# Kernel tuning notes

Measured on AMD Instinct MI355X. Metric: run time of the kernel, lower is better.

The kernel has to match this reference:

```python
import jax, jax.numpy as jnp
import numpy as np
from jax import lax

B, C, H, W = 4, 128, 64, 64
GC = 32        # branch channels = C * branch_ratio
DI = 64        # SS2D d_inner = 2 * GC (expand=2)
DT_RANK = 2    # ceil(GC / 16)


def _conv(x, w, pad, dilation=1, groups=1):
    return lax.conv_general_dilated(x, w, (1, 1), [(pad, pad), (pad, pad)],
                                    rhs_dilation=(dilation, dilation),
                                    feature_group_count=groups,
                                    dimension_numbers=('NCHW', 'OIHW', 'NCHW'))


def _bn(x, g, b, m, v):
    # inference-mode BatchNorm2d
    s = g / jnp.sqrt(v + 1e-5)
    return x * s[None, :, None, None] + (b - m * s)[None, :, None, None]


def _selective_scan(u, delta, A, Bm, Cm, D, dbias):
    # u, delta: (B,K,Di,L); A: (K,Di,N); Bm,Cm: (B,K,N,L); D,dbias: (K,Di)
    delta = jax.nn.softplus(delta + dbias[None, :, :, None])
    Bsz, K, Di, L = u.shape
    N = A.shape[-1]

    def step(h, inp):
        dt, bt, ct, ut = inp  # dt,ut: (B,K,Di); bt,ct: (B,K,N)
        h = jnp.exp(dt[..., None] * A) * h + (dt * ut)[..., None] * bt[:, :, None, :]
        return h, jnp.einsum('bkdn,bkn->bkd', h, ct)

    xs = (jnp.moveaxis(delta, -1, 0), jnp.moveaxis(Bm, -1, 0),
          jnp.moveaxis(Cm, -1, 0), jnp.moveaxis(u, -1, 0))
    _, ys = lax.scan(step, jnp.zeros((Bsz, K, Di, N), u.dtype), xs)
    return jnp.moveaxis(ys, 0, -1) + u * D[None, :, :, None]


def _ss2d(x, in_w, cw, cb, xp_w, dt_w, dt_b, A_log, Dp, ln_g, ln_b, out_w):
    # VMamba SS2D on NCHW input
    Bsz, Cc, Hh, Ww = x.shape
    di = in_w.shape[0] // 2
    dc = cw.shape[-1]
    xz = jnp.einsum('bchw,ec->behw', x, in_w)          # in_proj (bias=False)
    xi, z = jnp.split(xz, 2, axis=1)
    xc = jax.nn.silu(_conv(xi, cw, (dc - 1) // 2, groups=di) + cb[None, :, None, None])
    L = Hh * Ww
    xf = xc.reshape(Bsz, di, L)
    xt = xc.transpose(0, 1, 3, 2).reshape(Bsz, di, L)
    x2 = jnp.stack([xf, xt], 1)
    xs4 = jnp.concatenate([x2, jnp.flip(x2, -1)], 1)   # (B,4,di,L) cross-scan
    x_dbl = jnp.einsum('bkdl,kcd->bkcl', xs4, xp_w)
    r = dt_w.shape[-1]
    N = A_log.shape[-1]
    dts = jnp.einsum('bkrl,kdr->bkdl', x_dbl[:, :, :r], dt_w)
    Bs = x_dbl[:, :, r:r + N]
    Cs = x_dbl[:, :, r + N:]
    A = -jnp.exp(A_log).reshape(4, di, N)
    oy = _selective_scan(xs4, dts, A, Bs, Cs, Dp.reshape(4, di), dt_b)
    inv = jnp.flip(oy[:, 2:4], -1)
    wh = oy[:, 1].reshape(Bsz, di, Ww, Hh).transpose(0, 1, 3, 2).reshape(Bsz, di, L)
    iwh = inv[:, 1].reshape(Bsz, di, Ww, Hh).transpose(0, 1, 3, 2).reshape(Bsz, di, L)
    y = (oy[:, 0] + inv[:, 0] + wh + iwh).transpose(0, 2, 1).reshape(Bsz, Hh, Ww, di)
    mu = y.mean(-1, keepdims=True)
    y = (y - mu) * lax.rsqrt(((y - mu) ** 2).mean(-1, keepdims=True) + 1e-5) * ln_g + ln_b
    y = y * jax.nn.silu(z.transpose(0, 2, 3, 1))
    return jnp.einsum('bhwd,cd->bchw', y, out_w)


def _gcss2d(x, in_w, cw, cb, xp_w, dt_w, dt_b, A_log, Dp, ln_g, ln_b, out_w, pw, bg, bb, bm, bv):
    s = _ss2d(x, in_w, cw, cb, xp_w, dt_w, dt_b, A_log, Dp, ln_g, ln_b, out_w)
    # AdaptiveAvgPool2d(1) + bilinear upsample of a 1x1 map == broadcast
    pool = jnp.broadcast_to(x.mean((2, 3), keepdims=True), s.shape)
    return jax.nn.relu(_bn(_conv(jnp.concatenate([s, pool], 1), pw, 0), bg, bb, bm, bv))


def _forward(x, conv1_w, conv1_bn_g, conv1_bn_b, conv1_bn_m, conv1_bn_v,
             ss2_in_proj_w, ss2_conv_w, ss2_conv_b, ss2_x_proj_w, ss2_dt_w, ss2_dt_b,
             ss2_A_log, ss2_D, ss2_ln_g, ss2_ln_b, ss2_out_proj_w,
             g2_proj_w, g2_bn_g, g2_bn_b, g2_bn_m, g2_bn_v,
             conv3_w,
             ss4_in_proj_w, ss4_conv_w, ss4_conv_b, ss4_x_proj_w, ss4_dt_w, ss4_dt_b,
             ss4_A_log, ss4_D, ss4_ln_g, ss4_ln_b, ss4_out_proj_w,
             g4_proj_w, g4_bn_g, g4_bn_b, g4_bn_m, g4_bn_v,
             gp_w, proj_w, proj_bn_g, proj_bn_b, proj_bn_m, proj_bn_v,
             ca_w1, ca_b1, ca_w2, ca_b2, sa_w):
    Cc = x.shape[1]
    x1, x2, x3, x4 = jnp.split(x, [Cc - 3 * GC, Cc - 2 * GC, Cc - GC], axis=1)
    out1 = jax.nn.relu(_bn(_conv(x1, conv1_w, 1), conv1_bn_g, conv1_bn_b, conv1_bn_m, conv1_bn_v))
    out2 = _gcss2d(x2, ss2_in_proj_w, ss2_conv_w, ss2_conv_b, ss2_x_proj_w, ss2_dt_w,
                   ss2_dt_b, ss2_A_log, ss2_D, ss2_ln_g, ss2_ln_b, ss2_out_proj_w,
                   g2_proj_w, g2_bn_g, g2_bn_b, g2_bn_m, g2_bn_v)
    out3 = jax.nn.relu(_conv(x3 + x1, conv3_w, 12, dilation=12))
    out4 = _gcss2d(x4 + x2, ss4_in_proj_w, ss4_conv_w, ss4_conv_b, ss4_x_proj_w, ss4_dt_w,
                   ss4_dt_b, ss4_A_log, ss4_D, ss4_ln_g, ss4_ln_b, ss4_out_proj_w,
                   g4_proj_w, g4_bn_g, g4_bn_b, g4_bn_m, g4_bn_v)
    fused = jnp.concatenate([out1, out2, out3, out4], 1)
    gf = jax.nn.relu(_conv(x.mean((2, 3), keepdims=True), gp_w, 0))
    gf = jnp.broadcast_to(gf, fused.shape)
    y = jnp.concatenate([fused, gf], 1)
    y = x + jax.nn.relu(_bn(_conv(y, proj_w, 0), proj_bn_g, proj_bn_b, proj_bn_m, proj_bn_v))
    # RCSA (dropout is identity in eval)
    ca = jax.nn.sigmoid(
        _conv(jax.nn.relu(_conv(y.mean((2, 3), keepdims=True), ca_w1, 0)
                          + ca_b1[None, :, None, None]), ca_w2, 0)
        + ca_b2[None, :, None, None])
    sa = jax.nn.sigmoid(_conv(y, sa_w, 3))
    return y * (ca * sa) + y


def setup_inputs():
    key = jax.random.key(0)
    ctr = [0]

    def rn(shape, s=0.1):
        ctr[0] += 1
        return s * jax.random.normal(jax.random.fold_in(key, ctr[0]), shape, jnp.float32)

    def alog(n):
        # VMamba A init: log(1..N) per (direction*d_inner) row
        return jnp.tile(jnp.log(jnp.arange(1, n + 1, dtype=jnp.float32))[None], (4 * DI, 1))

    return dict(
        x=rn((B, C, H, W), 1.0),
        conv1_w=rn((GC, GC, 3, 3)),
        conv1_bn_g=jnp.ones(GC), conv1_bn_b=jnp.zeros(GC),
        conv1_bn_m=jnp.zeros(GC), conv1_bn_v=jnp.ones(GC),
        ss2_in_proj_w=rn((2 * DI, GC)),
        ss2_conv_w=rn((DI, 1, 3, 3)), ss2_conv_b=rn((DI,)),
        ss2_x_proj_w=rn((4, DT_RANK + 2 * 8, DI)),
        ss2_dt_w=rn((4, DI, DT_RANK)), ss2_dt_b=rn((4, DI)),
        ss2_A_log=alog(8), ss2_D=jnp.ones(4 * DI),
        ss2_ln_g=jnp.ones(DI), ss2_ln_b=jnp.zeros(DI),
        ss2_out_proj_w=rn((GC, DI)),
        g2_proj_w=rn((GC, 2 * GC, 1, 1)),
        g2_bn_g=jnp.ones(GC), g2_bn_b=jnp.zeros(GC), g2_bn_m=jnp.zeros(GC), g2_bn_v=jnp.ones(GC),
        conv3_w=rn((GC, GC, 3, 3)),
        ss4_in_proj_w=rn((2 * DI, GC)),
        ss4_conv_w=rn((DI, 1, 7, 7)), ss4_conv_b=rn((DI,)),
        ss4_x_proj_w=rn((4, DT_RANK + 2 * 24, DI)),
        ss4_dt_w=rn((4, DI, DT_RANK)), ss4_dt_b=rn((4, DI)),
        ss4_A_log=alog(24), ss4_D=jnp.ones(4 * DI),
        ss4_ln_g=jnp.ones(DI), ss4_ln_b=jnp.zeros(DI),
        ss4_out_proj_w=rn((GC, DI)),
        g4_proj_w=rn((GC, 2 * GC, 1, 1)),
        g4_bn_g=jnp.ones(GC), g4_bn_b=jnp.zeros(GC), g4_bn_m=jnp.zeros(GC), g4_bn_v=jnp.ones(GC),
        gp_w=rn((C, C, 1, 1)),
        proj_w=rn((C, 2 * C, 1, 1)),
        proj_bn_g=jnp.ones(C), proj_bn_b=jnp.zeros(C),
        proj_bn_m=jnp.zeros(C), proj_bn_v=jnp.ones(C),
        ca_w1=rn((C // 16, C, 1, 1)), ca_b1=jnp.zeros(C // 16),
        ca_w2=rn((C, C // 16, 1, 1)), ca_b2=jnp.zeros(C),
        sa_w=rn((1, C, 7, 7)),
    )


def reference(x, conv1_w, conv1_bn_g, conv1_bn_b, conv1_bn_m, conv1_bn_v,
              ss2_in_proj_w, ss2_conv_w, ss2_conv_b, ss2_x_proj_w, ss2_dt_w, ss2_dt_b,
              ss2_A_log, ss2_D, ss2_ln_g, ss2_ln_b, ss2_out_proj_w,
              g2_proj_w, g2_bn_g, g2_bn_b, g2_bn_m, g2_bn_v,
              conv3_w,
              ss4_in_proj_w, ss4_conv_w, ss4_conv_b, ss4_x_proj_w, ss4_dt_w, ss4_dt_b,
              ss4_A_log, ss4_D, ss4_ln_g, ss4_ln_b, ss4_out_proj_w,
              g4_proj_w, g4_bn_g, g4_bn_b, g4_bn_m, g4_bn_v,
              gp_w, proj_w, proj_bn_g, proj_bn_b, proj_bn_m, proj_bn_v,
              ca_w1, ca_b1, ca_w2, ca_b2, sa_w):
    return _forward(x, conv1_w, conv1_bn_g, conv1_bn_b, conv1_bn_m, conv1_bn_v,
                    ss2_in_proj_w, ss2_conv_w, ss2_conv_b, ss2_x_proj_w, ss2_dt_w, ss2_dt_b,
                    ss2_A_log, ss2_D, ss2_ln_g, ss2_ln_b, ss2_out_proj_w,
                    g2_proj_w, g2_bn_g, g2_bn_b, g2_bn_m, g2_bn_v,
                    conv3_w,
                    ss4_in_proj_w, ss4_conv_w, ss4_conv_b, ss4_x_proj_w, ss4_dt_w, ss4_dt_b,
                    ss4_A_log, ss4_D, ss4_ln_g, ss4_ln_b, ss4_out_proj_w,
                    g4_proj_w, g4_bn_g, g4_bn_b, g4_bn_m, g4_bn_v,
                    gp_w, proj_w, proj_bn_g, proj_bn_b, proj_bn_m, proj_bn_v,
                    ca_w1, ca_b1, ca_w2, ca_b2, sa_w)
```

## Files before the change

kernel.cpp:

```cpp
#include <hip/hip_runtime.h>
#include <math.h>

#define BB 4
#define CCH 128
#define LL 4096
#define LOG2E 1.44269504088896340736f

__device__ __forceinline__ float exp2fast(float x) {
    float r; asm("v_exp_f32 %0, %1" : "=v"(r) : "v"(x)); return r;
}
__device__ __forceinline__ float softplusf(float x) {
    return x > 20.f ? x : log1pf(expf(x));
}
__device__ __forceinline__ float sigmf(float x) {
    return 1.f / (1.f + expf(-x));
}

__device__ __forceinline__ int dirmap(int k, int l) {
    if (k == 0) return l;
    if (k == 1) return ((l & 63) << 6) | (l >> 6);
    if (k == 2) return LL - 1 - l;
    int j = LL - 1 - l; return ((j & 63) << 6) | (j >> 6);
}

__global__ void k_prepA(const float* __restrict__ Alog2, const float* __restrict__ Alog4,
                        float* __restrict__ A2_2, float* __restrict__ A2_4) {
    int i = blockIdx.x * 256 + threadIdx.x;
    if (i < 4 * 64 * 8)  A2_2[i] = -expf(Alog2[i]) * LOG2E;
    if (i < 4 * 64 * 24) A2_4[i] = -expf(Alog4[i]) * LOG2E;
}

__global__ void k_addgroups(const float* __restrict__ x, float* __restrict__ x13, float* __restrict__ x42) {
    int i = blockIdx.x * 256 + threadIdx.x;
    int l = i & (LL - 1); int c = (i >> 12) & 31; int b = i >> 17;
    const float* xb = x + (size_t)b * CCH * LL;
    x13[i] = xb[(64 + c) * LL + l] + xb[(0 + c) * LL + l];
    x42[i] = xb[(96 + c) * LL + l] + xb[(32 + c) * LL + l];
}

__global__ void k_pool(const float* __restrict__ src, float* __restrict__ dst) {
    int bc = blockIdx.x;
    const float* p = src + (size_t)bc * LL;
    float s = 0.f;
    for (int i = threadIdx.x; i < LL; i += 256) s += p[i];
    for (int m = 32; m >= 1; m >>= 1) s += __shfl_xor(s, m, 64);
    __shared__ float ws[4];
    if ((threadIdx.x & 63) == 0) ws[threadIdx.x >> 6] = s;
    __syncthreads();
    if (threadIdx.x == 0) dst[bc] = (ws[0] + ws[1] + ws[2] + ws[3]) * (1.f / LL);
}

__global__ __launch_bounds__(256) void k_conv1L(const float* __restrict__ x,
                        const float* __restrict__ w1,
                        const float* __restrict__ g, const float* __restrict__ bt,
                        const float* __restrict__ m, const float* __restrict__ v,
                        float* __restrict__ out1) {
    __shared__ float t[32][3][66];
    int b = blockIdx.x >> 6, h = blockIdx.x & 63;
    int lane = threadIdx.x & 63, wv = threadIdx.x >> 6;
    const float* xb = x + (size_t)b * CCH * LL;
    for (int i = threadIdx.x; i < 192; i += 256) {
        int ci = i / 6, rem = i % 6;
        t[ci][rem >> 1][(rem & 1) ? 65 : 0] = 0.f;
    }
    for (int i = threadIdx.x; i < 6144; i += 256) {
        int ci = i / 192, rem = i % 192;
        int r = rem >> 6, col = rem & 63;
        int hh = h + r - 1;
        t[ci][r][col + 1] = ((unsigned)hh < 64u) ? xb[ci * LL + hh * 64 + col] : 0.f;
    }
    __syncthreads();
    float a[8];
    #pragma unroll
    for (int j = 0; j < 8; j++) a[j] = 0.f;
    for (int ci = 0; ci < 32; ci++) {
        #pragma unroll
        for (int r = 0; r < 3; r++) {
            float v0 = t[ci][r][lane];
            float v1 = t[ci][r][lane + 1];
            float v2 = t[ci][r][lane + 2];
            #pragma unroll
            for (int j = 0; j < 8; j++) {
                const float* wp = w1 + ((wv * 8 + j) * 32 + ci) * 9 + r * 3;
                a[j] = fmaf(wp[0], v0, fmaf(wp[1], v1, fmaf(wp[2], v2, a[j])));
            }
        }
    }
    #pragma unroll
    for (int j = 0; j < 8; j++) {
        int co = wv * 8 + j;
        float sc = g[co] * rsqrtf(v[co] + 1e-5f);
        float bs = bt[co] - m[co] * sc;
        out1[(size_t)(b * 32 + co) * LL + h * 64 + lane] = fmaxf(fmaf(a[j], sc, bs), 0.f);
    }
}

__global__ __launch_bounds__(256) void k_conv3L(const float* __restrict__ x13,
                        const float* __restrict__ w3, float* __restrict__ out3) {
    __shared__ float t[32][3][88];
    int b = blockIdx.x >> 6, h = blockIdx.x & 63;
    int lane = threadIdx.x & 63, wv = threadIdx.x >> 6;
    const float* xb = x13 + (size_t)b * 32 * LL;
    for (int i = threadIdx.x; i < 2304; i += 256) {
        int ci = i / 72, rem = i % 72;
        int r = rem / 24, cz = rem % 24;
        t[ci][r][(cz < 12) ? cz : (cz + 64)] = 0.f;
    }
    for (int i = threadIdx.x; i < 6144; i += 256) {
        int ci = i / 192, rem = i % 192;
        int r = rem >> 6, col = rem & 63;
        int hh = h + (r - 1) * 12;
        t[ci][r][col + 12] = ((unsigned)hh < 64u) ? xb[ci * LL + hh * 64 + col] : 0.f;
    }
    __syncthreads();
    float a[8];
    #pragma unroll
    for (int j = 0; j < 8; j++) a[j] = 0.f;
    for (int ci = 0; ci < 32; ci++) {
        #pragma unroll
        for (int r = 0; r < 3; r++) {
            float v0 = t[ci][r][lane];
            float v1 = t[ci][r][lane + 12];
            float v2 = t[ci][r][lane + 24];
            #pragma unroll
            for (int j = 0; j < 8; j++) {
                const float* wp = w3 + ((wv * 8 + j) * 32 + ci) * 9 + r * 3;
                a[j] = fmaf(wp[0], v0, fmaf(wp[1], v1, fmaf(wp[2], v2, a[j])));
            }
        }
    }
    #pragma unroll
    for (int j = 0; j < 8; j++) {
        int co = wv * 8 + j;
        out3[(size_t)(b * 32 + co) * LL + h * 64 + lane] = fmaxf(a[j], 0.f);
    }
}

__global__ __launch_bounds__(256) void k_s1(const float* __restrict__ src, int bstride, int coff,
                     const float* __restrict__ in_w,
                     float* __restrict__ xiT, float* __restrict__ zT) {
    int blk = blockIdx.x;
    int l0 = (blk & 63) * 64; int b = blk >> 6;
    int lq = threadIdx.x & 63; int esub = threadIdx.x >> 6;
    __shared__ float xin[32][64];
    __shared__ float xit[64][65];
    __shared__ float zt[64][65];
    for (int i = threadIdx.x; i < 32 * 64; i += 256) {
        int c = i >> 6, q = i & 63;
        xin[c][q] = src[(size_t)b * bstride + (size_t)(coff + c) * LL + l0 + q];
    }
    __syncthreads();
    for (int it = 0; it < 32; it++) {
        int e = esub * 32 + it;
        const float* wr = in_w + e * 32;
        float acc = 0.f;
        #pragma unroll 8
        for (int c = 0; c < 32; c++) acc += wr[c] * xin[c][lq];
        if (e < 64) xit[lq][e] = acc;
        else        zt[lq][e - 64] = acc;
    }
    __syncthreads();
    for (int i = threadIdx.x; i < 64 * 64; i += 256) {
        int q = i >> 6, d = i & 63;
        size_t st = ((size_t)b * LL + l0 + q) * 64 + d;
        xiT[st] = xit[q][d];
        zT[st]  = zt[q][d];
    }
}

template<int K>
__global__ __launch_bounds__(256) void k_s2(const float* __restrict__ xiT, const float* __restrict__ cw,
                     const float* __restrict__ cb, float* __restrict__ xcT) {
    const int P = (K - 1) / 2;
    __shared__ float wl[64 * K * K];
    for (int j = threadIdx.x; j < 64 * K * K; j += 256) wl[j] = cw[j];
    __syncthreads();
    int g = blockIdx.x * 4 + (threadIdx.x >> 6);
    int d = threadIdx.x & 63;
    int l4 = g & 1023; int b = g >> 10;
    int l = l4 << 2;
    int h = l >> 6, w0 = l & 63;
    const float* xb = xiT + (size_t)b * LL * 64;
    const float* wp = wl + d * K * K;
    float bias = cb[d];
    float a0 = bias, a1 = bias, a2 = bias, a3 = bias;
    #pragma unroll
    for (int kh = 0; kh < K; kh++) {
        int hh = h + kh - P; if ((unsigned)hh >= 64u) continue;
        float val[K + 3];
        #pragma unroll
        for (int j = 0; j < K + 3; j++) {
            int w2 = w0 + j - P;
            val[j] = ((unsigned)w2 < 64u) ? xb[(size_t)(hh * 64 + w2) * 64 + d] : 0.f;
        }
        #pragma unroll
        for (int kw = 0; kw < K; kw++) {
            float wk = wp[kh * K + kw];
            a0 = fmaf(wk, val[kw], a0);
            a1 = fmaf(wk, val[kw + 1], a1);
            a2 = fmaf(wk, val[kw + 2], a2);
            a3 = fmaf(wk, val[kw + 3], a3);
        }
    }
    size_t ob = ((size_t)b * LL + l) * 64 + d;
    xcT[ob]            = a0 / (1.f + expf(-a0));
    xcT[ob + 64]       = a1 / (1.f + expf(-a1));
    xcT[ob + 128]      = a2 / (1.f + expf(-a2));
    xcT[ob + 192]      = a3 / (1.f + expf(-a3));
}

template<int N>
__global__ __launch_bounds__(256) void k_s3(const float* __restrict__ xcT, const float* __restrict__ xp_w,
                     float* __restrict__ r01, float* __restrict__ Bsb, float* __restrict__ Csb) {
    const int CD = 2 + 2 * N;
    int blk = blockIdx.x;
    int lt = blk & 255; int k = (blk >> 8) & 3; int b = blk >> 10;
    int l0 = lt * 16; int bk = b * 4 + k;
    __shared__ float xt[64][17];
    __shared__ float xp[CD * 64];
    __shared__ float accs[CD][16];
    for (int i = threadIdx.x; i < 64 * 16; i += 256) {
        int dd = i & 63, lq = i >> 6;
        xt[dd][lq] = xcT[((size_t)b * LL + dirmap(k, l0 + lq)) * 64 + dd];
    }
    for (int i = threadIdx.x; i < CD * 64; i += 256) xp[i] = xp_w[(size_t)k * CD * 64 + i];
    __syncthreads();
    for (int o = threadIdx.x; o < CD * 16; o += 256) {
        int cc = o >> 4, lq = o & 15;
        const float* wr = &xp[cc * 64];
        float acc = 0.f;
        #pragma unroll 8
        for (int dd = 0; dd < 64; dd++) acc += wr[dd] * xt[dd][lq];
        accs[cc][lq] = acc;
    }
    __syncthreads();
    for (int i = threadIdx.x; i < 32; i += 256) {
        int lq = i >> 1, j = i & 1;
        r01[((size_t)bk * LL + l0 + lq) * 2 + j] = accs[j][lq];
    }
    for (int i = threadIdx.x; i < 16 * N; i += 256) {
        int lq = i / N, n = i - lq * N;
        Bsb[((size_t)bk * LL + l0 + lq) * N + n] = accs[2 + n][lq];
        Csb[((size_t)bk * LL + l0 + lq) * N + n] = accs[2 + N + n][lq];
    }
}

template<int N>
__global__ __launch_bounds__(256) void k_scanA(
    const float* __restrict__ r01, const float* __restrict__ Bs,
    const float* __restrict__ xcT, const float* __restrict__ A2,
    const float* __restrict__ dtw, const float* __restrict__ dtb,
    float* __restrict__ Pp, float* __restrict__ Hl) {
    const int N4 = N / 4;
    __shared__ float2 dd2[32][64];
    __shared__ float lb[32 * N];
    int bk = blockIdx.x >> 7; int c = blockIdx.x & 127;
    int k = bk & 3, b = bk >> 2;
    int tid = threadIdx.x;
    int d = tid & 63, wv = tid >> 6;
    int l0 = c * 32;
    const float* Bp = Bs + ((size_t)bk * LL + l0) * N;
    for (int i = tid; i < 32 * N; i += 256) lb[i] = Bp[i];
    {
        float w0 = dtw[(k * 64 + d) * 2], w1 = dtw[(k * 64 + d) * 2 + 1], bd = dtb[k * 64 + d];
        const float2* rp = (const float2*)(r01 + (size_t)bk * LL * 2);
        const float* xb = xcT + (size_t)b * LL * 64;
        #pragma unroll
        for (int j = 0; j < 8; j++) {
            int t = wv * 8 + j;
            float2 rv = rp[l0 + t];
            float u = xb[(size_t)dirmap(k, l0 + t) * 64 + d];
            float dt = softplusf(fmaf(rv.x, w0, fmaf(rv.y, w1, bd)));
            dd2[t][d] = make_float2(dt, dt * u);
        }
    }
    __syncthreads();
    float a2[N4], h[N4], P[N4];
    #pragma unroll
    for (int n = 0; n < N4; n++) {
        a2[n] = A2[(k * 64 + d) * N + wv * N4 + n];
        h[n] = 0.f; P[n] = 1.f;
    }
    for (int t = 0; t < 32; t++) {
        float2 dv = dd2[t][d];
        const float* bl = &lb[t * N + wv * N4];
        #pragma unroll
        for (int n = 0; n < N4; n++) {
            float a = exp2fast(dv.x * a2[n]);
            P[n] *= a;
            h[n] = fmaf(a, h[n], dv.y * bl[n]);
        }
    }
    size_t o = (size_t)(bk * 128 + c) * N * 64 + d;
    #pragma unroll
    for (int n = 0; n < N4; n++) {
        Pp[o + (size_t)(wv * N4 + n) * 64] = P[n];
        Hl[o + (size_t)(wv * N4 + n) * 64] = h[n];
    }
}

template<int N>
__global__ void k_scanB(const float* __restrict__ Pp, float* __restrict__ Hl) {
    int g = blockIdx.x * 256 + threadIdx.x;
    if (g >= 16 * N * 64) return;
    int d = g & 63; int n = (g >> 6) % N; int bk = g / (N * 64);
    const size_t stride = (size_t)N * 64;
    size_t o = (size_t)bk * 128 * stride + n * 64 + d;
    float acc = 0.f;
    float Pv = Pp[o], Hv = Hl[o];
    for (int c = 0; c < 128; c++) {
        float Pn = 0.f, Hn = 0.f;
        if (c < 127) { Pn = Pp[o + stride]; Hn = Hl[o + stride]; }
        Hl[o] = acc;
        acc = fmaf(Pv, acc, Hv);
        Pv = Pn; Hv = Hn;
        o += stride;
    }
}

template<int N>
__global__ __launch_bounds__(256) void k_scanC(
    const float* __restrict__ r01, const float* __restrict__ Bs,
    const float* __restrict__ Cs, const float* __restrict__ xcT,
    const float* __restrict__ A2, const float* __restrict__ dtw,
    const float* __restrict__ dtb, const float* __restrict__ Hin,
    float* __restrict__ yrT) {
    const int N4 = N / 4;
    __shared__ float2 dd2[32][64];
    __shared__ float lb[32 * N];
    __shared__ float lc[32 * N];
    __shared__ float yacc[4][8][64];
    int bk = blockIdx.x >> 7; int c = blockIdx.x & 127;
    int k = bk & 3, b = bk >> 2;
    int tid = threadIdx.x;
    int d = tid & 63, wv = tid >> 6;
    int l0 = c * 32;
    const float* Bp = Bs + ((size_t)bk * LL + l0) * N;
    const float* Cp = Cs + ((size_t)bk * LL + l0) * N;
    for (int i = tid; i < 32 * N; i += 256) { lb[i] = Bp[i]; lc[i] = Cp[i]; }
    {
        float w0 = dtw[(k * 64 + d) * 2], w1 = dtw[(k * 64 + d) * 2 + 1], bd = dtb[k * 64 + d];
        const float2* rp = (const float2*)(r01 + (size_t)bk * LL * 2);
        const float* xb = xcT + (size_t)b * LL * 64;
        #pragma unroll
        for (int j = 0; j < 8; j++) {
            int t = wv * 8 + j;
            float2 rv = rp[l0 + t];
            float u = xb[(size_t)dirmap(k, l0 + t) * 64 + d];
            float dt = softplusf(fmaf(rv.x, w0, fmaf(rv.y, w1, bd)));
            dd2[t][d] = make_float2(dt, dt * u);
        }
    }
    float a2[N4], h[N4];
    size_t o = (size_t)(bk * 128 + c) * N * 64 + d;
    #pragma unroll
    for (int n = 0; n < N4; n++) {
        a2[n] = A2[(k * 64 + d) * N + wv * N4 + n];
        h[n] = Hin[o + (size_t)(wv * N4 + n) * 64];
    }
    __syncthreads();
    float* yo = yrT + (size_t)(k * BB + b) * LL * 64;
    for (int st = 0; st < 4; st++) {
        #pragma unroll
        for (int j = 0; j < 8; j++) {
            int t = st * 8 + j;
            float2 dv = dd2[t][d];
            const float* bl = &lb[t * N + wv * N4];
            const float* cl = &lc[t * N + wv * N4];
            float y = 0.f;
            #pragma unroll
            for (int n = 0; n < N4; n++) {
                float a = exp2fast(dv.x * a2[n]);
                h[n] = fmaf(a, h[n], dv.y * bl[n]);
                y = fmaf(h[n], cl[n], y);
            }
            yacc[wv][j][d] = y;
        }
        __syncthreads();
        for (int i = tid; i < 512; i += 256) {
            int j = i >> 6, q = i & 63;
            float y = yacc[0][j][q] + yacc[1][j][q] + yacc[2][j][q] + yacc[3][j][q];
            yo[(size_t)dirmap(k, l0 + st * 8 + j) * 64 + q] = y;
        }
        __syncthreads();
    }
}

__global__ __launch_bounds__(256) void k_combine(const float* __restrict__ yrT, const float* __restrict__ xcT,
                          const float* __restrict__ zT, const float* __restrict__ Dp,
                          const float* __restrict__ ln_g, const float* __restrict__ ln_b,
                          const float* __restrict__ out_w, float* __restrict__ sbuf) {
    int blk = blockIdx.x;
    int l0 = (blk & 127) * 32; int b = blk >> 7;
    int tid = threadIdx.x;
    __shared__ float yt[32][65];
    __shared__ float yg[32][65];
    __shared__ float muS[32], rsS[32];
    const size_t DS = (size_t)BB * LL * 64;
    for (int i = tid; i < 2048; i += 256) {
        int d = i & 63, q = i >> 6;
        size_t st = ((size_t)b * LL + l0 + q) * 64 + d;
        float yv = yrT[st] + yrT[DS + st] + yrT[2 * DS + st] + yrT[3 * DS + st];
        float sd = Dp[d] + Dp[64 + d] + Dp[128 + d] + Dp[192 + d];
        yt[q][d] = fmaf(xcT[st], sd, yv);
    }
    __syncthreads();
    {
        int q = tid >> 3, sub = tid & 7;
        float s = 0.f, sq = 0.f;
        #pragma unroll
        for (int j = 0; j < 8; j++) {
            float vv = yt[q][sub * 8 + j]; s += vv; sq = fmaf(vv, vv, sq);
        }
        #pragma unroll
        for (int m = 1; m < 8; m <<= 1) {
            s += __shfl_xor(s, m, 64); sq += __shfl_xor(sq, m, 64);
        }
        if (sub == 0) {
            float mm = s * (1.f / 64.f);
            muS[q] = mm;
            rsS[q] = rsqrtf(fmaf(sq, 1.f / 64.f, -mm * mm) + 1e-5f);
        }
    }
    __syncthreads();
    for (int i = tid; i < 2048; i += 256) {
        int d = i & 63, q = i >> 6;
        float gn = fmaf((yt[q][d] - muS[q]) * rsS[q], ln_g[d], ln_b[d]);
        float z = zT[((size_t)b * LL + l0 + q) * 64 + d];
        yg[q][d] = gn * z / (1.f + expf(-z));
    }
    __syncthreads();
    for (int i = tid; i < 32 * 32; i += 256) {
        int e = i >> 5, q = i & 31;
        const float* wr = out_w + e * 64;
        float acc = 0.f;
        #pragma unroll 8
        for (int d = 0; d < 64; d++) acc += wr[d] * yg[q][d];
        sbuf[((size_t)b * 32 + e) * LL + l0 + q] = acc;
    }
}

__global__ __launch_bounds__(256) void k_gtail(const float* __restrict__ sbuf, const float* __restrict__ pw,
                        const float* __restrict__ gfpool, int poolOff, int poolOff2,
                        const float* __restrict__ g, const float* __restrict__ bt,
                        const float* __restrict__ m, const float* __restrict__ v,
                        float* __restrict__ out) {
    int i = blockIdx.x * 256 + threadIdx.x;
    int l4 = i & 1023; int co = (i >> 10) & 31; int b = i >> 15;
    int l = l4 << 2;
    const float* pwr = pw + co * 64;
    float pacc = 0.f;
    #pragma unroll 8
    for (int c = 0; c < 32; c++) {
        float pv = gfpool[b * 128 + poolOff + c];
        if (poolOff2 >= 0) pv += gfpool[b * 128 + poolOff2 + c];
        pacc = fmaf(pwr[32 + c], pv, pacc);
    }
    float a0 = pacc, a1 = pacc, a2 = pacc, a3 = pacc;
    const float* sb = sbuf + (size_t)b * 32 * LL + l;
    #pragma unroll 8
    for (int c = 0; c < 32; c++) {
        float4 sv = *(const float4*)(sb + (size_t)c * LL);
        float wk = pwr[c];
        a0 = fmaf(wk, sv.x, a0);
        a1 = fmaf(wk, sv.y, a1);
        a2 = fmaf(wk, sv.z, a2);
        a3 = fmaf(wk, sv.w, a3);
    }
    float sc = g[co] * rsqrtf(v[co] + 1e-5f);
    float bs = bt[co] - m[co] * sc;
    float4 o;
    o.x = fmaxf(fmaf(a0, sc, bs), 0.f);
    o.y = fmaxf(fmaf(a1, sc, bs), 0.f);
    o.z = fmaxf(fmaf(a2, sc, bs), 0.f);
    o.w = fmaxf(fmaf(a3, sc, bs), 0.f);
    *(float4*)(out + (size_t)(b * 32 + co) * LL + l) = o;
}

__global__ void k_gf(const float* __restrict__ gfpool, const float* __restrict__ gp_w,
                     const float* __restrict__ proj_w, float* __restrict__ gf, float* __restrict__ pgf) {
    __shared__ float gfl[4][128];
    int t = threadIdx.x;
    int b = t >> 7, e = t & 127;
    float acc = 0.f;
    for (int c = 0; c < 128; c++) acc += gp_w[e * 128 + c] * gfpool[b * 128 + c];
    acc = fmaxf(acc, 0.f);
    gf[b * 128 + e] = acc; gfl[b][e] = acc;
    __syncthreads();
    float a2 = 0.f;
    for (int c = 0; c < 128; c++) a2 += proj_w[e * 256 + 128 + c] * gfl[b][c];
    pgf[b * 128 + e] = a2;
}

__global__ __launch_bounds__(256) void k_proj(const float* __restrict__ x,
                       const float* __restrict__ o1, const float* __restrict__ o2,
                       const float* __restrict__ o3, const float* __restrict__ o4,
                       const float* __restrict__ proj_w, const float* __restrict__ pgf,
                       const float* __restrict__ g, const float* __restrict__ bt,
                       const float* __restrict__ m, const float* __restrict__ v,
                       float* __restrict__ ybuf) {
    int i = blockIdx.x * 256 + threadIdx.x;
    int l4 = i & 1023; int cg = (i >> 10) & 31; int b = i >> 15;
    int l = l4 << 2; int co0 = cg << 2;
    float acc[4][4];
    #pragma unroll
    for (int j = 0; j < 4; j++) {
        float pg = pgf[b * 128 + co0 + j];
        #pragma unroll
        for (int q = 0; q < 4; q++) acc[j][q] = pg;
    }
    size_t ob = (size_t)b * 32 * LL + l;
    const float* wr = proj_w + co0 * 256;
    #pragma unroll 4
    for (int c = 0; c < 32; c++) {
        float4 vv = *(const float4*)(o1 + ob + (size_t)c * LL);
        #pragma unroll
        for (int j = 0; j < 4; j++) {
            float wk = wr[j * 256 + c];
            acc[j][0] = fmaf(wk, vv.x, acc[j][0]); acc[j][1] = fmaf(wk, vv.y, acc[j][1]);
            acc[j][2] = fmaf(wk, vv.z, acc[j][2]); acc[j][3] = fmaf(wk, vv.w, acc[j][3]);
        }
    }
    #pragma unroll 4
    for (int c = 0; c < 32; c++) {
        float4 vv = *(const float4*)(o2 + ob + (size_t)c * LL);
        #pragma unroll
        for (int j = 0; j < 4; j++) {
            float wk = wr[j * 256 + 32 + c];
            acc[j][0] = fmaf(wk, vv.x, acc[j][0]); acc[j][1] = fmaf(wk, vv.y, acc[j][1]);
            acc[j][2] = fmaf(wk, vv.z, acc[j][2]); acc[j][3] = fmaf(wk, vv.w, acc[j][3]);
        }
    }
    #pragma unroll 4
    for (int c = 0; c < 32; c++) {
        float4 vv = *(const float4*)(o3 + ob + (size_t)c * LL);
        #pragma unroll
        for (int j = 0; j < 4; j++) {
            float wk = wr[j * 256 + 64 + c];
            acc[j][0] = fmaf(wk, vv.x, acc[j][0]); acc[j][1] = fmaf(wk, vv.y, acc[j][1]);
            acc[j][2] = fmaf(wk, vv.z, acc[j][2]); acc[j][3] = fmaf(wk, vv.w, acc[j][3]);
        }
    }
    #pragma unroll 4
    for (int c = 0; c < 32; c++) {
        float4 vv = *(const float4*)(o4 + ob + (size_t)c * LL);
        #pragma unroll
        for (int j = 0; j < 4; j++) {
            float wk = wr[j * 256 + 96 + c];
            acc[j][0] = fmaf(wk, vv.x, acc[j][0]); acc[j][1] = fmaf(wk, vv.y, acc[j][1]);
            acc[j][2] = fmaf(wk, vv.z, acc[j][2]); acc[j][3] = fmaf(wk, vv.w, acc[j][3]);
        }
    }
    #pragma unroll
    for (int j = 0; j < 4; j++) {
        int co = co0 + j;
        float sc = g[co] * rsqrtf(v[co] + 1e-5f);
        float bs = bt[co] - m[co] * sc;
        float4 xv = *(const float4*)(x + (size_t)(b * 128 + co) * LL + l);
        float4 o;
        o.x = xv.x + fmaxf(fmaf(acc[j][0], sc, bs), 0.f);
        o.y = xv.y + fmaxf(fmaf(acc[j][1], sc, bs), 0.f);
        o.z = xv.z + fmaxf(fmaf(acc[j][2], sc, bs), 0.f);
        o.w = xv.w + fmaxf(fmaf(acc[j][3], sc, bs), 0.f);
        *(float4*)(ybuf + (size_t)(b * 128 + co) * LL + l) = o;
    }
}

__global__ void k_ca(const float* __restrict__ ypool, const float* __restrict__ w1,
                     const float* __restrict__ b1, const float* __restrict__ w2,
                     const float* __restrict__ b2, float* __restrict__ ca) {
    int b = blockIdx.x; int t = threadIdx.x;
    __shared__ float ym[128]; __shared__ float r1[8];
    ym[t] = ypool[b * 128 + t];
    __syncthreads();
    if (t < 8) {
        float a = b1[t];
        for (int c = 0; c < 128; c++) a += w1[t * 128 + c] * ym[c];
        r1[t] = fmaxf(a, 0.f);
    }
    __syncthreads();
    float a = b2[t];
    #pragma unroll
    for (int i2 = 0; i2 < 8; i2++) a += w2[t * 8 + i2] * r1[i2];
    ca[b * 128 + t] = sigmf(a);
}

__global__ __launch_bounds__(256) void k_sa_part(const float* __restrict__ ybuf, const float* __restrict__ sw,
                     float* __restrict__ pa) {
    __shared__ float wlds[16 * 49];
    __shared__ float rows[4][7][70];
    __shared__ float part[4][64];
    int cg = blockIdx.x & 7; int h = (blockIdx.x >> 3) & 63; int b = blockIdx.x >> 9;
    int lane = threadIdx.x & 63, wv = threadIdx.x >> 6;
    for (int i = threadIdx.x; i < 16 * 49; i += 256) wlds[i] = sw[cg * 16 * 49 + i];
    if (lane < 3) {
        #pragma unroll
        for (int r = 0; r < 7; r++) { rows[wv][r][lane] = 0.f; rows[wv][r][67 + lane] = 0.f; }
    }
    __syncthreads();
    float acc = 0.f;
    for (int it = 0; it < 4; it++) {
        int lc = it * 4 + wv; int c = cg * 16 + lc;
        const float* yp = ybuf + ((size_t)b * 128 + c) * LL;
        #pragma unroll
        for (int r = 0; r < 7; r++) {
            int hh = h + r - 3;
            rows[wv][r][3 + lane] = ((unsigned)hh < 64u) ? yp[hh * 64 + lane] : 0.f;
        }
        __syncthreads();
        const float* wp = wlds + lc * 49;
        #pragma unroll
        for (int kh = 0; kh < 7; kh++) {
            #pragma unroll
            for (int kw = 0; kw < 7; kw++) {
                acc = fmaf(wp[kh * 7 + kw], rows[wv][kh][lane + kw], acc);
            }
        }
        __syncthreads();
    }
    part[wv][lane] = acc;
    __syncthreads();
    if (threadIdx.x < 64) {
        float a = part[0][threadIdx.x] + part[1][threadIdx.x]
                + part[2][threadIdx.x] + part[3][threadIdx.x];
        pa[(size_t)cg * (BB * LL) + (size_t)b * LL + h * 64 + threadIdx.x] = a;
    }
}

__global__ void k_sared(const float* __restrict__ pa, float* __restrict__ sa) {
    int i = blockIdx.x * 256 + threadIdx.x;
    float s = 0.f;
    #pragma unroll
    for (int g = 0; g < 8; g++) s += pa[(size_t)g * (BB * LL) + i];
    sa[i] = sigmf(s);
}

__global__ void k_final(const float* __restrict__ ybuf, const float* __restrict__ ca,
                        const float* __restrict__ sa, float* __restrict__ out) {
    int i = blockIdx.x * 256 + threadIdx.x;
    int l = i & (LL - 1); int co = (i >> 12) & 127; int b = i >> 19;
    float y = ybuf[i];
    out[i] = y * (1.f + ca[b * 128 + co] * sa[b * 4096 + l]);
}

extern "C" void kernel_launch(void* const* d_in, const int* in_sizes, int n_in,
                              void* d_out, int out_size, void* d_ws, size_t ws_size,
                              hipStream_t stream) {
    const float* x        = (const float*)d_in[0];
    const float* conv1_w  = (const float*)d_in[1];
    const float* c1g = (const float*)d_in[2], *c1b = (const float*)d_in[3];
    const float* c1m = (const float*)d_in[4], *c1v = (const float*)d_in[5];
    const float* s2_inw   = (const float*)d_in[6];
    const float* s2_cw    = (const float*)d_in[7];
    const float* s2_cb    = (const float*)d_in[8];
    const float* s2_xpw   = (const float*)d_in[9];
    const float* s2_dtw   = (const float*)d_in[10];
    const float* s2_dtb   = (const float*)d_in[11];
    const float* s2_Alog  = (const float*)d_in[12];
    const float* s2_D     = (const float*)d_in[13];
    const float* s2_lng   = (const float*)d_in[14];
    const float* s2_lnb   = (const float*)d_in[15];
    const float* s2_outw  = (const float*)d_in[16];
    const float* g2_pw    = (const float*)d_in[17];
    const float* g2g = (const float*)d_in[18], *g2b = (const float*)d_in[19];
    const float* g2m = (const float*)d_in[20], *g2v = (const float*)d_in[21];
    const float* conv3_w  = (const float*)d_in[22];
    const float* s4_inw   = (const float*)d_in[23];
    const float* s4_cw    = (const float*)d_in[24];
    const float* s4_cb    = (const float*)d_in[25];
    const float* s4_xpw   = (const float*)d_in[26];
    const float* s4_dtw   = (const float*)d_in[27];
    const float* s4_dtb   = (const float*)d_in[28];
    const float* s4_Alog  = (const float*)d_in[29];
    const float* s4_D     = (const float*)d_in[30];
    const float* s4_lng   = (const float*)d_in[31];
    const float* s4_lnb   = (const float*)d_in[32];
    const float* s4_outw  = (const float*)d_in[33];
    const float* g4_pw    = (const float*)d_in[34];
    const float* g4g = (const float*)d_in[35], *g4b = (const float*)d_in[36];
    const float* g4m = (const float*)d_in[37], *g4v = (const float*)d_in[38];
    const float* gp_w     = (const float*)d_in[39];
    const float* proj_w   = (const float*)d_in[40];
    const float* pjg = (const float*)d_in[41], *pjb = (const float*)d_in[42];
    const float* pjm = (const float*)d_in[43], *pjv = (const float*)d_in[44];
    const float* ca_w1 = (const float*)d_in[45], *ca_b1 = (const float*)d_in[46];
    const float* ca_w2 = (const float*)d_in[47], *ca_b2 = (const float*)d_in[48];
    const float* sa_w  = (const float*)d_in[49];
    float* out = (float*)d_out;
    float* w = (float*)d_ws;

    const size_t o_out1 = 0;
    const size_t o_out2 = 524288;
    const size_t o_out3 = 1048576;
    const size_t o_out4 = 1572864;
    const size_t o_x42  = 2097152;
    const size_t o_gfp  = 2621440;
    const size_t o_gf   = 2621952;
    const size_t o_pgf  = 2622464;
    const size_t o_ypool= 2622976;
    const size_t o_ca   = 2623488;
    const size_t o_A2   = 2624000;
    const size_t o_A4   = 2626048;
    const size_t o_S    = 2632192;
    const size_t o_x13  = o_S;
    const size_t o_xiT  = o_S;
    const size_t o_Pp   = o_S;
    const size_t o_yrT  = o_S;
    const size_t o_ybuf = o_S;
    const size_t o_sa   = o_S + 2097152;
    const size_t o_sap  = o_S + 2113536;
    const size_t o_zT   = o_S + 4194304;
    const size_t o_xcT  = o_zT + 1048576;
    const size_t o_r01  = o_xcT + 1048576;
    const size_t o_Bs   = o_r01 + 131072;
    const size_t o_sbuf = o_Bs;
    const size_t o_Cs   = o_Bs + 1572864;
    const size_t o_Hl   = o_Cs + 1572864;

    dim3 b256(256);
    k_prepA<<<24, b256, 0, stream>>>(s2_Alog, s4_Alog, w + o_A2, w + o_A4);
    k_addgroups<<<2048, b256, 0, stream>>>(x, w + o_x13, w + o_x42);
    k_pool<<<512, b256, 0, stream>>>(x, w + o_gfp);
    k_conv1L<<<256, b256, 0, stream>>>(x, conv1_w, c1g, c1b, c1m, c1v, w + o_out1);
    k_conv3L<<<256, b256, 0, stream>>>(w + o_x13, conv3_w, w + o_out3);

    {
        const int N = 8;
        k_s1<<<256, b256, 0, stream>>>(x, CCH * LL, 32, s2_inw, w + o_xiT, w + o_zT);
        k_s2<3><<<1024, b256, 0, stream>>>(w + o_xiT, s2_cw, s2_cb, w + o_xcT);
        k_s3<N><<<4096, b256, 0, stream>>>(w + o_xcT, s2_xpw, w + o_r01, w + o_Bs, w + o_Cs);
        k_scanA<N><<<2048, b256, 0, stream>>>(w + o_r01, w + o_Bs, w + o_xcT, w + o_A2,
                                              s2_dtw, s2_dtb, w + o_Pp, w + o_Hl);
        k_scanB<N><<<(16 * N * 64 + 255) / 256, b256, 0, stream>>>(w + o_Pp, w + o_Hl);
        k_scanC<N><<<2048, b256, 0, stream>>>(w + o_r01, w + o_Bs, w + o_Cs, w + o_xcT,
                                              w + o_A2, s2_dtw, s2_dtb, w + o_Hl, w + o_yrT);
        k_combine<<<512, b256, 0, stream>>>(w + o_yrT, w + o_xcT, w + o_zT, s2_D,
                                            s2_lng, s2_lnb, s2_outw, w + o_sbuf);
        k_gtail<<<512, b256, 0, stream>>>(w + o_sbuf, g2_pw, w + o_gfp, 32, -1,
                                          g2g, g2b, g2m, g2v, w + o_out2);
    }
    {
        const int N = 24;
        k_s1<<<256, b256, 0, stream>>>(w + o_x42, 32 * LL, 0, s4_inw, w + o_xiT, w + o_zT);
        k_s2<7><<<1024, b256, 0, stream>>>(w + o_xiT, s4_cw, s4_cb, w + o_xcT);
        k_s3<N><<<4096, b256, 0, stream>>>(w + o_xcT, s4_xpw, w + o_r01, w + o_Bs, w + o_Cs);
        k_scanA<N><<<2048, b256, 0, stream>>>(w + o_r01, w + o_Bs, w + o_xcT, w + o_A4,
                                              s4_dtw, s4_dtb, w + o_Pp, w + o_Hl);
        k_scanB<N><<<(16 * N * 64 + 255) / 256, b256, 0, stream>>>(w + o_Pp, w + o_Hl);
        k_scanC<N><<<2048, b256, 0, stream>>>(w + o_r01, w + o_Bs, w + o_Cs, w + o_xcT,
                                              w + o_A4, s4_dtw, s4_dtb, w + o_Hl, w + o_yrT);
        k_combine<<<512, b256, 0, stream>>>(w + o_yrT, w + o_xcT, w + o_zT, s4_D,
                                            s4_lng, s4_lnb, s4_outw, w + o_sbuf);
        k_gtail<<<512, b256, 0, stream>>>(w + o_sbuf, g4_pw, w + o_gfp, 96, 32,
                                          g4g, g4b, g4m, g4v, w + o_out4);
    }

    k_gf<<<1, dim3(512), 0, stream>>>(w + o_gfp, gp_w, proj_w, w + o_gf, w + o_pgf);
    k_proj<<<512, b256, 0, stream>>>(x, w + o_out1, w + o_out2, w + o_out3, w + o_out4,
                                     proj_w, w + o_pgf, pjg, pjb, pjm, pjv, w + o_ybuf);
    k_pool<<<512, b256, 0, stream>>>(w + o_ybuf, w + o_ypool);
    k_ca<<<4, dim3(128), 0, stream>>>(w + o_ypool, ca_w1, ca_b1, ca_w2, ca_b2, w + o_ca);
    k_sa_part<<<2048, b256, 0, stream>>>(w + o_ybuf, sa_w, w + o_sap);
    k_sared<<<64, b256, 0, stream>>>(w + o_sap, w + o_sa);
    k_final<<<8192, b256, 0, stream>>>(w + o_ybuf, w + o_ca, w + o_sa, out);
}
```

Baseline: 578.5 us.

## Fold group adds into loaders, fuse out_proj with group tail, split chunk scan

Removes k_addgroups by summing the channel-group pairs directly inside the conv3 and s1 loads. The SS2D out_proj is pre-multiplied with the group projection and BN scale in a small prep kernel, so k_combine writes the final ReLU output and k_gtail plus its intermediate buffer go away. The serial 128-step inter-chunk scan becomes a three-pass hierarchical scan (16-chunk segments, a segment scan, then a fix-up pass) to expose more parallelism. In exchange it adds extra kernel launches and extra passes over Pp/Hl.

```diff
diff --git a/kernel.cpp b/kernel.cpp
--- a/kernel.cpp
+++ b/kernel.cpp
@@ -28,14 +28,6 @@
     int i = blockIdx.x * 256 + threadIdx.x;
     if (i < 4 * 64 * 8)  A2_2[i] = -expf(Alog2[i]) * LOG2E;
     if (i < 4 * 64 * 24) A2_4[i] = -expf(Alog4[i]) * LOG2E;
-}
-
-__global__ void k_addgroups(const float* __restrict__ x, float* __restrict__ x13, float* __restrict__ x42) {
-    int i = blockIdx.x * 256 + threadIdx.x;
-    int l = i & (LL - 1); int c = (i >> 12) & 31; int b = i >> 17;
-    const float* xb = x + (size_t)b * CCH * LL;
-    x13[i] = xb[(64 + c) * LL + l] + xb[(0 + c) * LL + l];
-    x42[i] = xb[(96 + c) * LL + l] + xb[(32 + c) * LL + l];
 }
 
 __global__ void k_pool(const float* __restrict__ src, float* __restrict__ dst) {
@@ -48,6 +40,33 @@
     if ((threadIdx.x & 63) == 0) ws[threadIdx.x >> 6] = s;
     __syncthreads();
     if (threadIdx.x == 0) dst[bc] = (ws[0] + ws[1] + ws[2] + ws[3]) * (1.f / LL);
+}
+
+__global__ void k_prepW(const float* __restrict__ pw, const float* __restrict__ outw,
+                        const float* __restrict__ g, const float* __restrict__ bt,
+                        const float* __restrict__ m, const float* __restrict__ v,
+                        const float* __restrict__ gfpool, int poolOff, int poolOff2,
+                        float* __restrict__ W2, float* __restrict__ pconst) {
+    int tid = threadIdx.x;
+    for (int i = tid; i < 2048; i += 256) {
+        int co = i >> 6, d = i & 63;
+        float s = 0.f;
+        #pragma unroll 8
+        for (int c = 0; c < 32; c++) s = fmaf(pw[co * 64 + c], outw[c * 64 + d], s);
+        float sc = g[co] * rsqrtf(v[co] + 1e-5f);
+        W2[i] = sc * s;
+    }
+    if (tid < 128) {
+        int b = tid >> 5, co = tid & 31;
+        float p = 0.f;
+        for (int c = 0; c < 32; c++) {
+            float pv = gfpool[b * 128 + poolOff + c];
+            if (poolOff2 >= 0) pv += gfpool[b * 128 + poolOff2 + c];
+            p = fmaf(pw[co * 64 + 32 + c], pv, p);
+        }
+        float sc = g[co] * rsqrtf(v[co] + 1e-5f);
+        pconst[tid] = fmaf(sc, p, bt[co] - m[co] * sc);
+    }
 }
 
 __global__ __launch_bounds__(256) void k_conv1L(const float* __restrict__ x,
@@ -95,12 +114,12 @@
     }
 }
 
-__global__ __launch_bounds__(256) void k_conv3L(const float* __restrict__ x13,
+__global__ __launch_bounds__(256) void k_conv3L(const float* __restrict__ x,
                         const float* __restrict__ w3, float* __restrict__ out3) {
     __shared__ float t[32][3][88];
     int b = blockIdx.x >> 6, h = blockIdx.x & 63;
     int lane = threadIdx.x & 63, wv = threadIdx.x >> 6;
-    const float* xb = x13 + (size_t)b * 32 * LL;
+    const float* xb = x + (size_t)b * CCH * LL;
     for (int i = threadIdx.x; i < 2304; i += 256) {
         int ci = i / 72, rem = i % 72;
         int r = rem / 24, cz = rem % 24;
@@ -110,7 +129,8 @@
         int ci = i / 192, rem = i % 192;
         int r = rem >> 6, col = rem & 63;
         int hh = h + (r - 1) * 12;
-        t[ci][r][col + 12] = ((unsigned)hh < 64u) ? xb[ci * LL + hh * 64 + col] : 0.f;
+        t[ci][r][col + 12] = ((unsigned)hh < 64u)
+            ? xb[ci * LL + hh * 64 + col] + xb[(64 + ci) * LL + hh * 64 + col] : 0.f;
     }
     __syncthreads();
     float a[8];
@@ -136,7 +156,7 @@
     }
 }
 
-__global__ __launch_bounds__(256) void k_s1(const float* __restrict__ src, int bstride, int coff,
+__global__ __launch_bounds__(256) void k_s1(const float* __restrict__ src, int coff, int coff2,
                      const float* __restrict__ in_w,
                      float* __restrict__ xiT, float* __restrict__ zT) {
     int blk = blockIdx.x;
@@ -147,7 +167,9 @@
     __shared__ float zt[64][65];
     for (int i = threadIdx.x; i < 32 * 64; i += 256) {
         int c = i >> 6, q = i & 63;
-        xin[c][q] = src[(size_t)b * bstride + (size_t)(coff + c) * LL + l0 + q];
+        float vv = src[(size_t)b * CCH * LL + (size_t)(coff + c) * LL + l0 + q];
+        if (coff2 >= 0) vv += src[(size_t)b * CCH * LL + (size_t)(coff2 + c) * LL + l0 + q];
+        xin[c][q] = vv;
     }
     __syncthreads();
     for (int it = 0; it < 32; it++) {
@@ -300,20 +322,54 @@
 }
 
 template<int N>
-__global__ void k_scanB(const float* __restrict__ Pp, float* __restrict__ Hl) {
+__global__ void k_scanB1(const float* __restrict__ Pp, const float* __restrict__ Hl,
+                         float* __restrict__ Psc, float* __restrict__ Hsc) {
+    int g = blockIdx.x * 256 + threadIdx.x;
+    if (g >= 16 * N * 512) return;
+    int d = g & 63; int sc = (g >> 6) & 7; int n = (g >> 9) % N; int bk = (g >> 9) / N;
+    const size_t stride = (size_t)N * 64;
+    size_t o = (size_t)(bk * 128 + sc * 16) * stride + n * 64 + d;
+    float P = 1.f, H = 0.f;
+    #pragma unroll 4
+    for (int c = 0; c < 16; c++) {
+        float Pv = Pp[o], Hv = Hl[o];
+        H = fmaf(Pv, H, Hv);
+        P *= Pv;
+        o += stride;
+    }
+    size_t sidx = ((size_t)(bk * 8 + sc) * N + n) * 64 + d;
+    Psc[sidx] = P; Hsc[sidx] = H;
+}
+
+template<int N>
+__global__ void k_scanB2(const float* __restrict__ Psc, float* __restrict__ Hsc) {
     int g = blockIdx.x * 256 + threadIdx.x;
     if (g >= 16 * N * 64) return;
-    int d = g & 63; int n = (g >> 6) % N; int bk = g / (N * 64);
+    int d = g & 63; int n = (g >> 6) % N; int bk = (g >> 6) / N;
+    float S = 0.f;
+    #pragma unroll
+    for (int sc = 0; sc < 8; sc++) {
+        size_t sidx = ((size_t)(bk * 8 + sc) * N + n) * 64 + d;
+        float Pv = Psc[sidx], Hv = Hsc[sidx];
+        Hsc[sidx] = S;
+        S = fmaf(Pv, S, Hv);
+    }
+}
+
+template<int N>
+__global__ void k_scanB3(const float* __restrict__ Pp, float* __restrict__ Hl,
+                         const float* __restrict__ Hsc) {
+    int g = blockIdx.x * 256 + threadIdx.x;
+    if (g >= 16 * N * 512) return;
+    int d = g & 63; int sc = (g >> 6) & 7; int n = (g >> 9) % N; int bk = (g >> 9) / N;
     const size_t stride = (size_t)N * 64;
-    size_t o = (size_t)bk * 128 * stride + n * 64 + d;
-    float acc = 0.f;
-    float Pv = Pp[o], Hv = Hl[o];
-    for (int c = 0; c < 128; c++) {
-        float Pn = 0.f, Hn = 0.f;
-        if (c < 127) { Pn = Pp[o + stride]; Hn = Hl[o + stride]; }
-        Hl[o] = acc;
-        acc = fmaf(Pv, acc, Hv);
-        Pv = Pn; Hv = Hn;
+    size_t o = (size_t)(bk * 128 + sc * 16) * stride + n * 64 + d;
+    float S = Hsc[((size_t)(bk * 8 + sc) * N + n) * 64 + d];
+    #pragma unroll 4
+    for (int c = 0; c < 16; c++) {
+        float Pv = Pp[o], Hv = Hl[o];
+        Hl[o] = S;
+        S = fmaf(Pv, S, Hv);
         o += stride;
     }
 }
@@ -389,7 +445,8 @@
 __global__ __launch_bounds__(256) void k_combine(const float* __restrict__ yrT, const float* __restrict__ xcT,
                           const float* __restrict__ zT, const float* __restrict__ Dp,
                           const float* __restrict__ ln_g, const float* __restrict__ ln_b,
-                          const float* __restrict__ out_w, float* __restrict__ sbuf) {
+                          const float* __restrict__ W2, const float* __restrict__ pconst,
+                          float* __restrict__ outg) {
     int blk = blockIdx.x;
     int l0 = (blk & 127) * 32; int b = blk >> 7;
     int tid = threadIdx.x;
@@ -432,49 +489,12 @@
     __syncthreads();
     for (int i = tid; i < 32 * 32; i += 256) {
         int e = i >> 5, q = i & 31;
-        const float* wr = out_w + e * 64;
-        float acc = 0.f;
+        const float* wr = W2 + e * 64;
+        float acc = pconst[b * 32 + e];
         #pragma unroll 8
         for (int d = 0; d < 64; d++) acc += wr[d] * yg[q][d];
-        sbuf[((size_t)b * 32 + e) * LL + l0 + q] = acc;
-    }
-}
-
-__global__ __launch_bounds__(256) void k_gtail(const float* __restrict__ sbuf, const float* __restrict__ pw,
-                        const float* __restrict__ gfpool, int poolOff, int poolOff2,
-                        const float* __restrict__ g, const float* __restrict__ bt,
-                        const float* __restrict__ m, const float* __restrict__ v,
-                        float* __restrict__ out) {
-    int i = blockIdx.x * 256 + threadIdx.x;
-    int l4 = i & 1023; int co = (i >> 10) & 31; int b = i >> 15;
-    int l = l4 << 2;
-    const float* pwr = pw + co * 64;
-    float pacc = 0.f;
-    #pragma unroll 8
-    for (int c = 0; c < 32; c++) {
-        float pv = gfpool[b * 128 + poolOff + c];
-        if (poolOff2 >= 0) pv += gfpool[b * 128 + poolOff2 + c];
-        pacc = fmaf(pwr[32 + c], pv, pacc);
-    }
-    float a0 = pacc, a1 = pacc, a2 = pacc, a3 = pacc;
-    const float* sb = sbuf + (size_t)b * 32 * LL + l;
-    #pragma unroll 8
-    for (int c = 0; c < 32; c++) {
-        float4 sv = *(const float4*)(sb + (size_t)c * LL);
-        float wk = pwr[c];
-        a0 = fmaf(wk, sv.x, a0);
-        a1 = fmaf(wk, sv.y, a1);
-        a2 = fmaf(wk, sv.z, a2);
-        a3 = fmaf(wk, sv.w, a3);
-    }
-    float sc = g[co] * rsqrtf(v[co] + 1e-5f);
-    float bs = bt[co] - m[co] * sc;
-    float4 o;
-    o.x = fmaxf(fmaf(a0, sc, bs), 0.f);
-    o.y = fmaxf(fmaf(a1, sc, bs), 0.f);
-    o.z = fmaxf(fmaf(a2, sc, bs), 0.f);
-    o.w = fmaxf(fmaf(a3, sc, bs), 0.f);
-    *(float4*)(out + (size_t)(b * 32 + co) * LL + l) = o;
+        outg[((size_t)b * 32 + e) * LL + l0 + q] = fmaxf(acc, 0.f);
+    }
 }
 
 __global__ void k_gf(const float* __restrict__ gfpool, const float* __restrict__ gp_w,
@@ -693,7 +713,10 @@
     const size_t o_out2 = 524288;
     const size_t o_out3 = 1048576;
     const size_t o_out4 = 1572864;
-    const size_t o_x42  = 2097152;
+    const size_t o_W2a  = 2097152;
+    const size_t o_W2b  = 2099200;
+    const size_t o_pc2  = 2101248;
+    const size_t o_pc4  = 2101376;
     const size_t o_gfp  = 2621440;
     const size_t o_gf   = 2621952;
     const size_t o_pgf  = 2622464;
@@ -702,7 +725,6 @@
     const size_t o_A2   = 2624000;
     const size_t o_A4   = 2626048;
     const size_t o_S    = 2632192;
-    const size_t o_x13  = o_S;
     const size_t o_xiT  = o_S;
     const size_t o_Pp   = o_S;
     const size_t o_yrT  = o_S;
@@ -713,46 +735,54 @@
     const size_t o_xcT  = o_zT + 1048576;
     const size_t o_r01  = o_xcT + 1048576;
     const size_t o_Bs   = o_r01 + 131072;
-    const size_t o_sbuf = o_Bs;
     const size_t o_Cs   = o_Bs + 1572864;
     const size_t o_Hl   = o_Cs + 1572864;
+    const size_t o_Psc  = 15346176;
+    const size_t o_Hsc  = o_Psc + 786432;
 
     dim3 b256(256);
     k_prepA<<<24, b256, 0, stream>>>(s2_Alog, s4_Alog, w + o_A2, w + o_A4);
-    k_addgroups<<<2048, b256, 0, stream>>>(x, w + o_x13, w + o_x42);
     k_pool<<<512, b256, 0, stream>>>(x, w + o_gfp);
+    k_prepW<<<1, b256, 0, stream>>>(g2_pw, s2_outw, g2g, g2b, g2m, g2v,
+                                    w + o_gfp, 32, -1, w + o_W2a, w + o_pc2);
+    k_prepW<<<1, b256, 0, stream>>>(g4_pw, s4_outw, g4g, g4b, g4m, g4v,
+                                    w + o_gfp, 96, 32, w + o_W2b, w + o_pc4);
     k_conv1L<<<256, b256, 0, stream>>>(x, conv1_w, c1g, c1b, c1m, c1v, w + o_out1);
-    k_conv3L<<<256, b256, 0, stream>>>(w + o_x13, conv3_w, w + o_out3);
+    k_conv3L<<<256, b256, 0, stream>>>(x, conv3_w, w + o_out3);
 
     {
         const int N = 8;
-        k_s1<<<256, b256, 0, stream>>>(x, CCH * LL, 32, s2_inw, w + o_xiT, w + o_zT);
+        k_s1<<<256, b256, 0, stream>>>(x, 32, -1, s2_inw, w + o_xiT, w + o_zT);
         k_s2<3><<<1024, b256, 0, stream>>>(w + o_xiT, s2_cw, s2_cb, w + o_xcT);
         k_s3<N><<<4096, b256, 0, stream>>>(w + o_xcT, s2_xpw, w + o_r01, w + o_Bs, w + o_Cs);
         k_scanA<N><<<2048, b256, 0, stream>>>(w + o_r01, w + o_Bs, w + o_xcT, w + o_A2,
                                               s2_dtw, s2_dtb, w + o_Pp, w + o_Hl);
-        k_scanB<N><<<(16 * N * 64 + 255) / 256, b256, 0, stream>>>(w + o_Pp, w + o_Hl);
+        k_scanB1<N><<<(16 * N * 512 + 255) / 256, b256, 0, stream>>>(w + o_Pp, w + o_Hl,
+                                                                     w + o_Psc, w + o_Hsc);
+        k_scanB2<N><<<(16 * N * 64 + 255) / 256, b256, 0, stream>>>(w + o_Psc, w + o_Hsc);
+        k_scanB3<N><<<(16 * N * 512 + 255) / 256, b256, 0, stream>>>(w + o_Pp, w + o_Hl,
+                                                                     w + o_Hsc);
         k_scanC<N><<<2048, b256, 0, stream>>>(w + o_r01, w + o_Bs, w + o_Cs, w + o_xcT,
                                               w + o_A2, s2_dtw, s2_dtb, w + o_Hl, w + o_yrT);
         k_combine<<<512, b256, 0, stream>>>(w + o_yrT, w + o_xcT, w + o_zT, s2_D,
-                                            s2_lng, s2_lnb, s2_outw, w + o_sbuf);
-        k_gtail<<<512, b256, 0, stream>>>(w + o_sbuf, g2_pw, w + o_gfp, 32, -1,
-                                          g2g, g2b, g2m, g2v, w + o_out2);
+                                            s2_lng, s2_lnb, w + o_W2a, w + o_pc2, w + o_out2);
     }
     {
         const int N = 24;
-        k_s1<<<256, b256, 0, stream>>>(w + o_x42, 32 * LL, 0, s4_inw, w + o_xiT, w + o_zT);
+        k_s1<<<256, b256, 0, stream>>>(x, 96, 32, s4_inw, w + o_xiT, w + o_zT);
         k_s2<7><<<1024, b256, 0, stream>>>(w + o_xiT, s4_cw, s4_cb, w + o_xcT);
         k_s3<N><<<4096, b256, 0, stream>>>(w + o_xcT, s4_xpw, w + o_r01, w + o_Bs, w + o_Cs);
         k_scanA<N><<<2048, b256, 0, stream>>>(w + o_r01, w + o_Bs, w + o_xcT, w + o_A4,
                                               s4_dtw, s4_dtb, w + o_Pp, w + o_Hl);
-        k_scanB<N><<<(16 * N * 64 + 255) / 256, b256, 0, stream>>>(w + o_Pp, w + o_Hl);
+        k_scanB1<N><<<(16 * N * 512 + 255) / 256, b256, 0, stream>>>(w + o_Pp, w + o_Hl,
+                                                                     w + o_Psc, w + o_Hsc);
+        k_scanB2<N><<<(16 * N * 64 + 255) / 256, b256, 0, stream>>>(w + o_Psc, w + o_Hsc);
+        k_scanB3<N><<<(16 * N * 512 + 255) / 256, b256, 0, stream>>>(w + o_Pp, w + o_Hl,
+                                                                     w + o_Hsc);
         k_scanC<N><<<2048, b256, 0, stream>>>(w + o_r01, w + o_Bs, w + o_Cs, w + o_xcT,
                                               w + o_A4, s4_dtw, s4_dtb, w + o_Hl, w + o_yrT);
         k_combine<<<512, b256, 0, stream>>>(w + o_yrT, w + o_xcT, w + o_zT, s4_D,
-                                            s4_lng, s4_lnb, s4_outw, w + o_sbuf);
-        k_gtail<<<512, b256, 0, stream>>>(w + o_sbuf, g4_pw, w + o_gfp, 96, 32,
-                                          g4g, g4b, g4m, g4v, w + o_out4);
+                                            s4_lng, s4_lnb, w + o_W2b, w + o_pc4, w + o_out4);
     }
 
     k_gf<<<1, dim3(512), 0, stream>>>(w + o_gfp, gp_w, proj_w, w + o_gf, w + o_pgf);
```

After: 581.8 us. No clear change (+0.6%).
